# Kernel optimization log

Hardware: AMD Instinct MI355X
Metric: run time of the kernel (lower is better)

The kernel has to match this reference:

```python
import jax, jax.numpy as jnp
import numpy as np

VOCAB, EMB, HID, LAT = 32000, 512, 1024, 64
B, S = 64, 512

def setup_inputs() -> dict:
    key = jax.random.key(0)
    ks = jax.random.split(key, 10)
    s_e = 1.0 / np.sqrt(HID)
    s_l = 1.0 / np.sqrt(HID)
    return {
        'input_ids': jax.random.randint(ks[0], (B, S), 0, VOCAB),
        'emb_weight': jax.random.normal(ks[1], (VOCAB, EMB), jnp.float32),
        'w_ih': jax.random.uniform(ks[2], (3 * HID, EMB), jnp.float32, -s_e, s_e),
        'w_hh': jax.random.uniform(ks[3], (3 * HID, HID), jnp.float32, -s_e, s_e),
        'b_ih': jax.random.uniform(ks[4], (3 * HID,), jnp.float32, -s_e, s_e),
        'b_hh': jax.random.uniform(ks[5], (3 * HID,), jnp.float32, -s_e, s_e),
        'w_mean': jax.random.uniform(ks[6], (LAT, HID), jnp.float32, -s_l, s_l),
        'b_mean': jax.random.uniform(ks[7], (LAT,), jnp.float32, -s_l, s_l),
        'w_logv': jax.random.uniform(ks[8], (LAT, HID), jnp.float32, -s_l, s_l),
        'b_logv': jax.random.uniform(ks[9], (LAT,), jnp.float32, -s_l, s_l),
    }

def _gru_mean_hidden(ids, emb_weight, w_ih, w_hh, b_ih, b_hh):
    x = emb_weight[ids]                      # [B, S, E]
    # precompute input-side gate preactivations for all timesteps
    gx = jnp.einsum('bse,ge->bsg', x, w_ih) + b_ih   # [B, S, 3H]
    gx_t = jnp.swapaxes(gx, 0, 1)            # [S, B, 3H] for scan

    def step(h, gx_i):
        gh = h @ w_hh.T + b_hh               # [B, 3H]
        # torch GRU gate order: r, z, n
        r = jax.nn.sigmoid(gx_i[:, :HID] + gh[:, :HID])
        z = jax.nn.sigmoid(gx_i[:, HID:2 * HID] + gh[:, HID:2 * HID])
        n = jnp.tanh(gx_i[:, 2 * HID:] + r * gh[:, 2 * HID:])
        h_new = (1.0 - z) * n + z * h
        return h_new, h_new

    h0 = jnp.zeros((ids.shape[0], HID), gx.dtype)
    _, hs = jax.lax.scan(step, h0, gx_t)      # hs: [S, B, H]
    return jnp.mean(hs, axis=0)               # mean pooling over time -> [B, H]

def reference(input_ids, emb_weight, w_ih, w_hh, b_ih, b_hh, w_mean, b_mean, w_logv, b_logv):
    h = _gru_mean_hidden(input_ids, emb_weight, w_ih, w_hh, b_ih, b_hh)
    mean = h @ w_mean.T + b_mean
    logv = h @ w_logv.T + b_logv
    return (mean, logv)
```

## Files before the change

### kernel.cpp

```cpp
#include <hip/hip_runtime.h>
#include <hip/hip_bf16.h>
#include <stdint.h>
#include <stddef.h>

#define HID   1024
#define NB    64
#define SEQ   512
#define G3    3072
#define EMB   512
#define LAT   64

typedef __attribute__((ext_vector_type(4))) float f32x4;
typedef __attribute__((ext_vector_type(8))) short bfrag;
typedef unsigned long long ull;

__device__ __forceinline__ unsigned short f2bf(float x) {
  union { float f; unsigned u; } v; v.f = x;
  unsigned u = v.u + 0x7fffu + ((v.u >> 16) & 1u);
  return (unsigned short)(u >> 16);
}
__device__ __forceinline__ float bf2f(short s) {
  union { unsigned u; float f; } v; v.u = ((unsigned)(unsigned short)s) << 16;
  return v.f;
}
__device__ __forceinline__ float fsig(float x) {
  return 1.0f / (1.0f + __builtin_exp2f(-1.4426950408889634f * x));
}
__device__ __forceinline__ float ftanh(float x) {
  return 1.0f - 2.0f / (1.0f + __builtin_exp2f(2.8853900817779268f * x));
}
__device__ __forceinline__ void gload_lds16(const void* g, void* l) {
  __builtin_amdgcn_global_load_lds(
      (const __attribute__((address_space(1))) unsigned int*)g,
      (__attribute__((address_space(3))) unsigned int*)l, 16, 0, 0);
}

__global__ void cvt_wih_kernel(const float* __restrict__ in, short* __restrict__ out) {
  int i = (blockIdx.x * 256 + threadIdx.x) * 8;
  f32x4 a = *(const f32x4*)(in + i);
  f32x4 b = *(const f32x4*)(in + i + 4);
  bfrag o;
  o[0]=(short)f2bf(a[0]); o[1]=(short)f2bf(a[1]); o[2]=(short)f2bf(a[2]); o[3]=(short)f2bf(a[3]);
  o[4]=(short)f2bf(b[0]); o[5]=(short)f2bf(b[1]); o[6]=(short)f2bf(b[2]); o[7]=(short)f2bf(b[3]);
  *(bfrag*)(out + i) = o;
}

__global__ void __launch_bounds__(256) gemm_gx_kernel(
    const int* __restrict__ ids, const float* __restrict__ emb,
    const short* __restrict__ wih, short* __restrict__ gx)
{
  const int nt = blockIdx.x, mt = blockIdx.y;
  const int tid = threadIdx.x;
  const int lane = tid & 63, wave = tid >> 6;
  const int wr = wave >> 1, wc = wave & 1;

  __shared__ __align__(16) short A_lds[128 * 48];
  __shared__ __align__(16) short B_lds[128 * 32];
  __shared__ int ids_s[128];

  if (tid < 128) ids_s[tid] = ids[mt * 128 + tid];
  __syncthreads();

  f32x4 acc[4][4];
  #pragma unroll
  for (int i = 0; i < 4; ++i)
    #pragma unroll
    for (int j = 0; j < 4; ++j) acc[i][j] = (f32x4){0.f, 0.f, 0.f, 0.f};

  const int r_stage = tid >> 1;
  const int kh = (tid & 1) * 16;

  #pragma unroll 1
  for (int kc = 0; kc < 16; ++kc) {
    __syncthreads();
    {
      const float* src = emb + (size_t)ids_s[r_stage] * 512 + kc * 32 + kh;
      f32x4 v0 = *(const f32x4*)(src);
      f32x4 v1 = *(const f32x4*)(src + 4);
      f32x4 v2 = *(const f32x4*)(src + 8);
      f32x4 v3 = *(const f32x4*)(src + 12);
      bfrag p0, p1;
      p0[0]=(short)f2bf(v0[0]); p0[1]=(short)f2bf(v0[1]); p0[2]=(short)f2bf(v0[2]); p0[3]=(short)f2bf(v0[3]);
      p0[4]=(short)f2bf(v1[0]); p0[5]=(short)f2bf(v1[1]); p0[6]=(short)f2bf(v1[2]); p0[7]=(short)f2bf(v1[3]);
      p1[0]=(short)f2bf(v2[0]); p1[1]=(short)f2bf(v2[1]); p1[2]=(short)f2bf(v2[2]); p1[3]=(short)f2bf(v2[3]);
      p1[4]=(short)f2bf(v3[0]); p1[5]=(short)f2bf(v3[1]); p1[6]=(short)f2bf(v3[2]); p1[7]=(short)f2bf(v3[3]);
      *(bfrag*)&A_lds[r_stage * 48 + kh]     = p0;
      *(bfrag*)&A_lds[r_stage * 48 + kh + 8] = p1;
    }
    {
      #pragma unroll
      for (int ii = 0; ii < 2; ++ii) {
        int i = wave * 2 + ii;
        const short* src = wih + (size_t)(nt * 128 + i * 16 + (lane >> 2)) * 512
                               + kc * 32 + (lane & 3) * 8;
        gload_lds16((const void*)src, (void*)&B_lds[i * 512]);
      }
    }
    asm volatile("s_waitcnt vmcnt(0)" ::: "memory");
    __syncthreads();

    bfrag a[4], b[4];
    #pragma unroll
    for (int mi = 0; mi < 4; ++mi)
      a[mi] = *(const bfrag*)&A_lds[(wr * 64 + mi * 16 + (lane & 15)) * 48 + (lane >> 4) * 8];
    #pragma unroll
    for (int ni = 0; ni < 4; ++ni)
      b[ni] = *(const bfrag*)&B_lds[(wc * 64 + ni * 16 + (lane & 15)) * 32 + (lane >> 4) * 8];
    #pragma unroll
    for (int mi = 0; mi < 4; ++mi)
      #pragma unroll
      for (int ni = 0; ni < 4; ++ni)
        acc[mi][ni] = __builtin_amdgcn_mfma_f32_16x16x32_bf16(a[mi], b[ni], acc[mi][ni], 0, 0, 0);
  }

  #pragma unroll
  for (int mi = 0; mi < 4; ++mi)
    #pragma unroll
    for (int ni = 0; ni < 4; ++ni)
      #pragma unroll
      for (int r = 0; r < 4; ++r) {
        int m = mt * 128 + wr * 64 + mi * 16 + (lane >> 4) * 4 + r;
        int n = nt * 128 + wc * 64 + ni * 16 + (lane & 15);
        gx[(size_t)m * G3 + n] = (short)f2bf(acc[mi][ni][r]);
      }
}

__global__ void __launch_bounds__(256, 1) gru_scan_kernel(
    const short* __restrict__ gx, const float* __restrict__ whh,
    const float* __restrict__ bihp, const float* __restrict__ bhhp,
    ull* __restrict__ hbuf_q, unsigned int* __restrict__ flags,
    float* __restrict__ hsum)
{
  const int wg   = blockIdx.x;
  const int team = wg >> 6;
  const int cg   = wg & 63;
  const int tid  = threadIdx.x;
  const int lane = tid & 63, wave = tid >> 6;
  const int bl   = lane & 15;
  const int bsub = (lane >> 4) * 4;
  const int jcol = cg * 16 + bl;
  const int bteam = team * 16;

  __shared__ __align__(16) short h_lds[16 * 1024];
  __shared__ __align__(16) float part[3 * 3 * 256];
  __shared__ __align__(16) short hstg[256];

  bfrag wfrag[3][8];
  #pragma unroll
  for (int g = 0; g < 3; ++g) {
    const float* wrow = whh + (size_t)(g * 1024 + jcol) * 1024 + wave * 256 + (lane >> 4) * 8;
    #pragma unroll
    for (int ks = 0; ks < 8; ++ks) {
      const float* p = wrow + ks * 32;
      f32x4 lo = *(const f32x4*)p;
      f32x4 hi = *(const f32x4*)(p + 4);
      bfrag f;
      f[0]=(short)f2bf(lo[0]); f[1]=(short)f2bf(lo[1]); f[2]=(short)f2bf(lo[2]); f[3]=(short)f2bf(lo[3]);
      f[4]=(short)f2bf(hi[0]); f[5]=(short)f2bf(hi[1]); f[6]=(short)f2bf(hi[2]); f[7]=(short)f2bf(hi[3]);
      wfrag[g][ks] = f;
    }
  }
  float bih_r[3], bhh_r[3];
  #pragma unroll
  for (int g = 0; g < 3; ++g) {
    bih_r[g] = bihp[g * 1024 + jcol];
    bhh_r[g] = bhhp[g * 1024 + jcol];
  }

  float hprev[4] = {0.f, 0.f, 0.f, 0.f};
  float hacc[4]  = {0.f, 0.f, 0.f, 0.f};
  const int xorm = (bl & 7) << 4;
  const char* lbase = (const char*)h_lds + bl * 2048;
  unsigned int* fteam = flags + team * 1024;
  unsigned int* myflag = fteam + cg * 16;

  short gxr_[4][3];
  if (wave == 0) {
    #pragma unroll
    for (int r = 0; r < 4; ++r) {
      size_t base = ((size_t)(bteam + bsub + r) * SEQ + 0) * G3 + jcol;
      gxr_[r][0] = gx[base];
      gxr_[r][1] = gx[base + 1024];
      gxr_[r][2] = gx[base + 2048];
    }
  }

  #pragma unroll 1
  for (int s = 0; s < SEQ; ++s) {
    const ull* hsrc = hbuf_q + ((s & 1) ? 16384 : 0) + team * 4096;
    ull*       hdst = hbuf_q + (((s + 1) & 1) ? 16384 : 0) + team * 4096;

    {
      ull hv[16];
      #pragma unroll
      for (int j = 0; j < 16; ++j)
        hv[j] = __hip_atomic_load(hsrc + j * 256 + tid, __ATOMIC_RELAXED,
                                  __HIP_MEMORY_SCOPE_AGENT);
      #pragma unroll
      for (int j = 0; j < 16; ++j) {
        int q  = j * 256 + tid;
        int cgq = q >> 6, b = (q >> 2) & 15, cq = q & 3;
        *(ull*)((char*)h_lds + b * 2048 + ((cgq * 32 + cq * 8) ^ ((b & 7) << 4))) = hv[j];
      }
    }
    __syncthreads();

    f32x4 a0 = {0.f,0.f,0.f,0.f}, a1 = {0.f,0.f,0.f,0.f}, a2 = {0.f,0.f,0.f,0.f};
    #pragma unroll
    for (int ks = 0; ks < 8; ++ks) {
      int k2 = wave * 512 + ks * 64 + (lane >> 4) * 16;
      bfrag af = *(const bfrag*)(lbase + (k2 ^ xorm));
      a0 = __builtin_amdgcn_mfma_f32_16x16x32_bf16(af, wfrag[0][ks], a0, 0, 0, 0);
      a1 = __builtin_amdgcn_mfma_f32_16x16x32_bf16(af, wfrag[1][ks], a1, 0, 0, 0);
      a2 = __builtin_amdgcn_mfma_f32_16x16x32_bf16(af, wfrag[2][ks], a2, 0, 0, 0);
    }
    if (wave) {
      int w1 = wave - 1;
      *(f32x4*)&part[((0 * 3 + w1) * 64 + lane) * 4] = a0;
      *(f32x4*)&part[((1 * 3 + w1) * 64 + lane) * 4] = a1;
      *(f32x4*)&part[((2 * 3 + w1) * 64 + lane) * 4] = a2;
    }
    __syncthreads();

    if (wave == 0) {
      f32x4 s0 = a0, s1 = a1, s2 = a2;
      #pragma unroll
      for (int w1 = 0; w1 < 3; ++w1) {
        s0 += *(const f32x4*)&part[((0 * 3 + w1) * 64 + lane) * 4];
        s1 += *(const f32x4*)&part[((1 * 3 + w1) * 64 + lane) * 4];
        s2 += *(const f32x4*)&part[((2 * 3 + w1) * 64 + lane) * 4];
      }
      #pragma unroll
      for (int r = 0; r < 4; ++r) {
        float ghr = s0[r] + bhh_r[0];
        float ghz = s1[r] + bhh_r[1];
        float ghn = s2[r] + bhh_r[2];
        float rg = fsig(bf2f(gxr_[r][0]) + bih_r[0] + ghr);
        float zg = fsig(bf2f(gxr_[r][1]) + bih_r[1] + ghz);
        float ng = ftanh(bf2f(gxr_[r][2]) + bih_r[2] + rg * ghn);
        float hn = (1.f - zg) * ng + zg * hprev[r];
        hprev[r] = hn;
        hacc[r] += hn;
        hstg[(bsub + r) * 16 + bl] = (short)f2bf(hn);
      }
    }
    __syncthreads();

    if (wave == 1) {
      ull v = ((const ull*)hstg)[lane];
      __hip_atomic_store(hdst + cg * 64 + lane, v, __ATOMIC_RELAXED,
                         __HIP_MEMORY_SCOPE_AGENT);
      asm volatile("s_waitcnt vmcnt(0)" ::: "memory");
      if (lane == 0)
        __hip_atomic_store(myflag, (unsigned)(s + 1), __ATOMIC_RELAXED,
                           __HIP_MEMORY_SCOPE_AGENT);
    }
    if (wave == 0) {
      int sn = (s + 1 < SEQ) ? (s + 1) : s;
      #pragma unroll
      for (int r = 0; r < 4; ++r) {
        size_t base = ((size_t)(bteam + bsub + r) * SEQ + sn) * G3 + jcol;
        gxr_[r][0] = gx[base];
        gxr_[r][1] = gx[base + 1024];
        gxr_[r][2] = gx[base + 2048];
      }
      unsigned tgt = (unsigned)(s + 1);
      for (;;) {
        unsigned v = __hip_atomic_load(fteam + lane * 16, __ATOMIC_RELAXED,
                                       __HIP_MEMORY_SCOPE_AGENT);
        if (__all((int)(v >= tgt))) break;
      }
    }
    __syncthreads();
  }

  if (wave == 0) {
    #pragma unroll
    for (int r = 0; r < 4; ++r)
      hsum[(size_t)(bteam + bsub + r) * 1024 + jcol] = hacc[r] * (1.0f / 512.0f);
  }
}

__global__ void proj_kernel(const float* __restrict__ hbar,
                            const float* __restrict__ wm, const float* __restrict__ bm,
                            const float* __restrict__ wl, const float* __restrict__ bl,
                            float* __restrict__ out)
{
  int b = blockIdx.x, t = threadIdx.x;
  __shared__ float hrow[1024];
  for (int k = t; k < 1024; k += 128) hrow[k] = hbar[(size_t)b * 1024 + k];
  __syncthreads();
  int j = t & 63;
  const float* w = (t < 64) ? (wm + (size_t)j * 1024) : (wl + (size_t)j * 1024);
  float acc = (t < 64) ? bm[j] : bl[j];
  for (int k = 0; k < 1024; k += 4) {
    f32x4 wv = *(const f32x4*)(w + k);
    acc += hrow[k] * wv[0] + hrow[k+1] * wv[1] + hrow[k+2] * wv[2] + hrow[k+3] * wv[3];
  }
  out[(size_t)((t < 64) ? 0 : 4096) + b * 64 + j] = acc;
}

extern "C" void kernel_launch(void* const* d_in, const int* in_sizes, int n_in,
                              void* d_out, int out_size, void* d_ws, size_t ws_size,
                              hipStream_t stream) {
  const int*   ids   = (const int*)d_in[0];
  const float* emb   = (const float*)d_in[1];
  const float* w_ih  = (const float*)d_in[2];
  const float* w_hh  = (const float*)d_in[3];
  const float* b_ih  = (const float*)d_in[4];
  const float* b_hh  = (const float*)d_in[5];
  const float* w_mean= (const float*)d_in[6];
  const float* b_mean= (const float*)d_in[7];
  const float* w_logv= (const float*)d_in[8];
  const float* b_logv= (const float*)d_in[9];
  float* out = (float*)d_out;

  char* ws = (char*)d_ws;
  unsigned int* flags = (unsigned int*)(ws);
  ull* hbuf_q        = (ull*)(ws + 16384);
  float* hsum        = (float*)(ws + 16384 + 262144);
  short* wihb        = (short*)(ws + 16384 + 262144 + 262144);
  short* gxbuf       = (short*)(ws + 16384 + 262144 + 262144 + 3145728);

  hipMemsetAsync(ws, 0, 16384 + 262144, stream);

  cvt_wih_kernel<<<768, 256, 0, stream>>>(w_ih, wihb);
  gemm_gx_kernel<<<dim3(24, 256), 256, 0, stream>>>(ids, emb, wihb, gxbuf);
  gru_scan_kernel<<<256, 256, 0, stream>>>(gxbuf, w_hh, b_ih, b_hh, hbuf_q, flags, hsum);
  proj_kernel<<<64, 128, 0, stream>>>(hsum, w_mean, b_mean, w_logv, b_logv, out);
}
```

Measured before the change: 2.031 ms.

## Replace flag-based cross-block barrier with epoch-tagged hidden-state words

Drops the separate per-block flag array and the spin-wait on flags. Each 64-bit hidden-state word now holds three bf16 values plus the step number in its top 16 bits. Consumers poll the data words directly until every tag matches the current step. This removes the store-drain wait, the flag store and a block barrier from the critical path of each timestep. In exchange the exchange buffer grows by half and consumers do more loads and repacking before writing LDS.

```diff
diff --git a/kernel.cpp b/kernel.cpp
--- a/kernel.cpp
+++ b/kernel.cpp
@@ -128,8 +128,7 @@
 __global__ void __launch_bounds__(256, 1) gru_scan_kernel(
     const short* __restrict__ gx, const float* __restrict__ whh,
     const float* __restrict__ bihp, const float* __restrict__ bhhp,
-    ull* __restrict__ hbuf_q, unsigned int* __restrict__ flags,
-    float* __restrict__ hsum)
+    ull* __restrict__ hbuf_q, float* __restrict__ hsum)
 {
   const int wg   = blockIdx.x;
   const int team = wg >> 6;
@@ -171,8 +170,6 @@
   float hacc[4]  = {0.f, 0.f, 0.f, 0.f};
   const int xorm = (bl & 7) << 4;
   const char* lbase = (const char*)h_lds + bl * 2048;
-  unsigned int* fteam = flags + team * 1024;
-  unsigned int* myflag = fteam + cg * 16;
 
   short gxr_[4][3];
   if (wave == 0) {
@@ -187,23 +184,61 @@
 
   #pragma unroll 1
   for (int s = 0; s < SEQ; ++s) {
-    const ull* hsrc = hbuf_q + ((s & 1) ? 16384 : 0) + team * 4096;
-    ull*       hdst = hbuf_q + (((s + 1) & 1) ? 16384 : 0) + team * 4096;
+    const ull* hsrc = hbuf_q + ((s & 1) ? 24576 : 0) + team * 6144;
+    ull*       hdst = hbuf_q + (((s + 1) & 1) ? 24576 : 0) + team * 6144;
 
     {
-      ull hv[16];
-      #pragma unroll
-      for (int j = 0; j < 16; ++j)
-        hv[j] = __hip_atomic_load(hsrc + j * 256 + tid, __ATOMIC_RELAXED,
-                                  __HIP_MEMORY_SCOPE_AGENT);
-      #pragma unroll
-      for (int j = 0; j < 16; ++j) {
-        int q  = j * 256 + tid;
-        int cgq = q >> 6, b = (q >> 2) & 15, cq = q & 3;
-        *(ull*)((char*)h_lds + b * 2048 + ((cgq * 32 + cq * 8) ^ ((b & 7) << 4))) = hv[j];
-      }
-    }
-    __syncthreads();
+      ull w[4][6];
+      #pragma unroll
+      for (int p = 0; p < 4; ++p) {
+        int P   = p * 64 + lane;
+        int cgq = wave * 16 + (P >> 4);
+        int b   = P & 15;
+        const ull* q = hsrc + cgq * 96 + b * 6;
+        #pragma unroll
+        for (int j = 0; j < 6; ++j)
+          w[p][j] = __hip_atomic_load(q + j, __ATOMIC_RELAXED,
+                                      __HIP_MEMORY_SCOPE_AGENT);
+      }
+      const ull want = (ull)(unsigned)s;
+      for (;;) {
+        int bad = 0;
+        #pragma unroll
+        for (int p = 0; p < 4; ++p) {
+          int P   = p * 64 + lane;
+          int cgq = wave * 16 + (P >> 4);
+          int b   = P & 15;
+          const ull* q = hsrc + cgq * 96 + b * 6;
+          #pragma unroll
+          for (int j = 0; j < 6; ++j)
+            if ((w[p][j] >> 48) != want) {
+              w[p][j] = __hip_atomic_load(q + j, __ATOMIC_RELAXED,
+                                          __HIP_MEMORY_SCOPE_AGENT);
+              bad = 1;
+            }
+        }
+        if (!bad) break;
+      }
+      #pragma unroll
+      for (int p = 0; p < 4; ++p) {
+        int P   = p * 64 + lane;
+        int cgq = wave * 16 + (P >> 4);
+        int b   = P & 15;
+        char* rowb = (char*)h_lds + b * 2048;
+        int swz = (b & 7) << 4;
+        #pragma unroll
+        for (int c4 = 0; c4 < 4; ++c4) {
+          ull u = 0;
+          #pragma unroll
+          for (int t = 0; t < 4; ++t) {
+            int c = c4 * 4 + t;
+            ull sh = (w[p][c / 3] >> ((c % 3) * 16)) & 0xFFFFull;
+            u |= sh << (t * 16);
+          }
+          *(ull*)(rowb + ((cgq * 32 + c4 * 8) ^ swz)) = u;
+        }
+      }
+    }
 
     f32x4 a0 = {0.f,0.f,0.f,0.f}, a1 = {0.f,0.f,0.f,0.f}, a2 = {0.f,0.f,0.f,0.f};
     #pragma unroll
@@ -247,13 +282,22 @@
     __syncthreads();
 
     if (wave == 1) {
-      ull v = ((const ull*)hstg)[lane];
-      __hip_atomic_store(hdst + cg * 64 + lane, v, __ATOMIC_RELAXED,
-                         __HIP_MEMORY_SCOPE_AGENT);
-      asm volatile("s_waitcnt vmcnt(0)" ::: "memory");
-      if (lane == 0)
-        __hip_atomic_store(myflag, (unsigned)(s + 1), __ATOMIC_RELAXED,
-                           __HIP_MEMORY_SCOPE_AGENT);
+      ull epv = (ull)(unsigned)(s + 1) << 48;
+      #pragma unroll
+      for (int rnd = 0; rnd < 2; ++rnd) {
+        int q = rnd * 64 + lane;
+        if (q < 96) {
+          int b  = q / 6;
+          int j  = q - b * 6;
+          int c0 = 3 * j;
+          ull v0 = (ull)(unsigned short)hstg[b * 16 + c0];
+          ull v1 = (c0 + 1 < 16) ? (ull)(unsigned short)hstg[b * 16 + c0 + 1] : 0ull;
+          ull v2 = (c0 + 2 < 16) ? (ull)(unsigned short)hstg[b * 16 + c0 + 2] : 0ull;
+          ull pq = v0 | (v1 << 16) | (v2 << 32) | epv;
+          __hip_atomic_store(hdst + cg * 96 + q, pq, __ATOMIC_RELAXED,
+                             __HIP_MEMORY_SCOPE_AGENT);
+        }
+      }
     }
     if (wave == 0) {
       int sn = (s + 1 < SEQ) ? (s + 1) : s;
@@ -264,14 +308,7 @@
         gxr_[r][1] = gx[base + 1024];
         gxr_[r][2] = gx[base + 2048];
       }
-      unsigned tgt = (unsigned)(s + 1);
-      for (;;) {
-        unsigned v = __hip_atomic_load(fteam + lane * 16, __ATOMIC_RELAXED,
-                                       __HIP_MEMORY_SCOPE_AGENT);
-        if (__all((int)(v >= tgt))) break;
-      }
-    }
-    __syncthreads();
+    }
   }
 
   if (wave == 0) {
@@ -316,16 +353,15 @@
   float* out = (float*)d_out;
 
   char* ws = (char*)d_ws;
-  unsigned int* flags = (unsigned int*)(ws);
-  ull* hbuf_q        = (ull*)(ws + 16384);
-  float* hsum        = (float*)(ws + 16384 + 262144);
-  short* wihb        = (short*)(ws + 16384 + 262144 + 262144);
-  short* gxbuf       = (short*)(ws + 16384 + 262144 + 262144 + 3145728);
-
-  hipMemsetAsync(ws, 0, 16384 + 262144, stream);
+  ull* hbuf_q   = (ull*)(ws);
+  float* hsum   = (float*)(ws + 393216);
+  short* wihb   = (short*)(ws + 393216 + 262144);
+  short* gxbuf  = (short*)(ws + 393216 + 262144 + 3145728);
+
+  hipMemsetAsync(ws, 0, 393216, stream);
 
   cvt_wih_kernel<<<768, 256, 0, stream>>>(w_ih, wihb);
   gemm_gx_kernel<<<dim3(24, 256), 256, 0, stream>>>(ids, emb, wihb, gxbuf);
-  gru_scan_kernel<<<256, 256, 0, stream>>>(gxbuf, w_hh, b_ih, b_hh, hbuf_q, flags, hsum);
+  gru_scan_kernel<<<256, 256, 0, stream>>>(gxbuf, w_hh, b_ih, b_hh, hbuf_q, hsum);
   proj_kernel<<<64, 128, 0, stream>>>(hsum, w_mean, b_mean, w_logv, b_logv, out);
 }
```

Measured after the change: 4.512 ms. +122.1%, slower.
